# Kernel optimization log

Measured on AMD Instinct MI355X. Metric: run time of the kernel, lower is better.

The kernel has to match this reference:

```python
import jax, jax.numpy as jnp
import numpy as np
from functools import partial

TAU = 2.0
V_TH = 1.0
T_STEPS = 10
SG_ALPHA = 4.0  # spikingjelly surrogate.Sigmoid default

@jax.custom_vjp
def spike(x):
    # Heaviside: 1 where x >= 0 (spikingjelly heaviside semantics)
    return (x >= 0).astype(x.dtype)

def _spike_fwd(x):
    return spike(x), x

def _spike_bwd(x, g):
    s = jax.nn.sigmoid(SG_ALPHA * x)
    return (g * SG_ALPHA * s * (1.0 - s),)

spike.defvjp(_spike_fwd, _spike_bwd)

def setup_inputs() -> dict:
    key = jax.random.key(0)
    ks = jax.random.split(key, 7)
    B, D_IN, H, A = 4096, 2048, 2048, 5
    def lin(k, fan_in, shape):
        bound = 1.0 / np.sqrt(fan_in)
        return jax.random.uniform(k, shape, jnp.float32, -bound, bound)
    return {
        "x": jax.random.normal(ks[0], (B, D_IN), jnp.float32),
        "W_in": lin(ks[1], D_IN, (D_IN, H)),
        "b_in": lin(ks[2], D_IN, (H,)),
        "W_snn": lin(ks[3], H, (H, H)),
        "b_snn": lin(ks[4], H, (H,)),
        "W_out": lin(ks[5], H, (H, A)),
        "b_out": lin(ks[6], H, (A,)),
    }

def lif_step(v, cur):
    # decay_input=True, v_reset=0: v <- v + (I - v)/tau; hard reset with detached spike
    v = v + (cur - v) / TAU
    s = spike(v - V_TH)
    v = (1.0 - jax.lax.stop_gradient(s)) * v
    return v, s

def reference(x, W_in, b_in, W_snn, b_snn, W_out, b_out):
    # input projection [B, H]
    h = x @ W_in + b_in
    # RSNNBlock: fc(h) is the same every timestep; LIF state carries across T steps
    cur = h @ W_snn + b_snn
    v0 = jnp.zeros_like(cur)
    _, spikes = jax.lax.scan(lambda v, _: lif_step(v, cur), v0, None, length=T_STEPS)
    rate = spikes.mean(axis=0)  # [B, H], mean firing rate
    # output head + single-step output LIF (fresh state v=0)
    pre = rate @ W_out + b_out  # [B, A]
    v_out, s_out = lif_step(jnp.zeros_like(pre), pre)
    return s_out
```

## Files before the change

### kernel.cpp

```cpp
#include <hip/hip_runtime.h>
#include <hip/hip_bf16.h>

static constexpr int BATCH = 4096;
static constexpr int DIN   = 2048;
static constexpr int HDIM  = 2048;
static constexpr int ADIM  = 5;

typedef __attribute__((ext_vector_type(8))) short short8;
typedef __attribute__((ext_vector_type(4))) float floatx4;

__device__ __forceinline__ unsigned short f2bf(float f) {
  unsigned int u = __float_as_uint(f);
  unsigned int r = (u + 0x7fffu + ((u >> 16) & 1u)) >> 16;
  return (unsigned short)r;
}
__device__ __forceinline__ float bf2f(unsigned short u) {
  return __uint_as_float(((unsigned int)u) << 16);
}

__global__ __launch_bounds__(256) void k_prep(const float* __restrict__ x,
                                              const float* __restrict__ W_in,
                                              const float* __restrict__ W_snn,
                                              unsigned short* __restrict__ xb,
                                              unsigned short* __restrict__ WinT,
                                              unsigned short* __restrict__ WsnT) {
  __shared__ float tl[32][33];
  const int b = blockIdx.x;
  if (b < 8192) {
    const int i = b * 256 + threadIdx.x;
    float4 v = ((const float4*)x)[i];
    ushort4 o;
    o.x = f2bf(v.x); o.y = f2bf(v.y); o.z = f2bf(v.z); o.w = f2bf(v.w);
    ((ushort4*)xb)[i] = o;
  } else {
    int bi = b - 8192;
    const float* src;
    unsigned short* dst;
    if (bi < 4096) { src = W_in; dst = WinT; }
    else           { src = W_snn; dst = WsnT; bi -= 4096; }
    const int bx = bi & 63, by = bi >> 6;
    const int c0 = bx * 32, r0 = by * 32;
    const int tx = threadIdx.x & 31, ty = threadIdx.x >> 5;
    #pragma unroll
    for (int s = 0; s < 32; s += 8)
      tl[ty + s][tx] = src[(size_t)(r0 + ty + s) * 2048 + (c0 + tx)];
    __syncthreads();
    #pragma unroll
    for (int s = 0; s < 32; s += 8)
      dst[(size_t)(c0 + ty + s) * 2048 + (r0 + tx)] = f2bf(tl[tx][ty + s]);
  }
}

template <int MODE>
__global__ __launch_bounds__(256, 2) void k_gemm(const unsigned short* __restrict__ Ag,
                                                 const unsigned short* __restrict__ BTg,
                                                 const float* __restrict__ bias,
                                                 unsigned short* __restrict__ outb,
                                                 int M, int N, int K) {
  constexpr int BK = 64;
  __shared__ unsigned short smem[2][16384];

  const int nbn = N / 128;
  const int nwg = gridDim.x;
  const int wg  = blockIdx.x;
  const int cpx = nwg >> 3;
  const int swz = (wg & 7) * cpx + (wg >> 3);
  const int bm = swz / nbn, bn = swz % nbn;
  const int m0 = bm * 128, n0 = bn * 128;

  const int t = threadIdx.x;
  const int l = t & 63;
  const int w = t >> 6;
  const int wc  = w & 1;
  const int kkh = w >> 1;

  const int srow = t >> 3;
  const int sg = (((t & 7) ^ (srow & 7)) << 3);
  const unsigned short* gA = Ag + (size_t)(m0 + srow) * K + sg;
  const unsigned short* gB = BTg + (size_t)(n0 + srow) * K + sg;

  const int NT = K / BK;

  auto stage = [&](int tt) {
    const int kt = tt * BK;
    char* base = (char*)&smem[tt & 1][0];
    #pragma unroll
    for (int j = 0; j < 4; ++j)
      __builtin_amdgcn_global_load_lds(
          (const __attribute__((address_space(1))) void*)(gA + (size_t)j * 32 * K + kt),
          (__attribute__((address_space(3))) void*)(base + t * 16 + j * 4096), 16, 0, 0);
    #pragma unroll
    for (int j = 0; j < 4; ++j)
      __builtin_amdgcn_global_load_lds(
          (const __attribute__((address_space(1))) void*)(gB + (size_t)j * 32 * K + kt),
          (__attribute__((address_space(3))) void*)(base + 16384 + t * 16 + j * 4096), 16, 0, 0);
  };

  const int soff = (((kkh << 2) | (l >> 4)) ^ (l & 7)) << 4;
  const int rA0 = (l & 15) * 128;
  const int rB0 = (wc * 64 + (l & 15)) * 128;

  floatx4 acc[8][4] = {};

  stage(0);
  __syncthreads();

  for (int tt = 0; tt < NT; ++tt) {
    if (tt + 1 < NT) stage(tt + 1);
    const char* Ab = (const char*)&smem[tt & 1][0];
    const char* Bb = Ab + 32768;
    short8 bf[4];
    #pragma unroll
    for (int j = 0; j < 4; ++j)
      bf[j] = *(const short8*)(Bb + rB0 + j * 2048 + soff);
    {
      short8 af[4];
      #pragma unroll
      for (int i = 0; i < 4; ++i)
        af[i] = *(const short8*)(Ab + rA0 + i * 2048 + soff);
      #pragma unroll
      for (int i = 0; i < 4; ++i)
        #pragma unroll
        for (int j = 0; j < 4; ++j)
          acc[i][j] = __builtin_amdgcn_mfma_f32_16x16x32_bf16(af[i], bf[j],
                                                              acc[i][j], 0, 0, 0);
    }
    {
      short8 af[4];
      #pragma unroll
      for (int i = 0; i < 4; ++i)
        af[i] = *(const short8*)(Ab + rA0 + (i + 4) * 2048 + soff);
      #pragma unroll
      for (int i = 0; i < 4; ++i)
        #pragma unroll
        for (int j = 0; j < 4; ++j)
          acc[i + 4][j] = __builtin_amdgcn_mfma_f32_16x16x32_bf16(af[i], bf[j],
                                                                  acc[i + 4][j], 0, 0, 0);
    }
    __syncthreads();
  }

  floatx4* xch = (floatx4*)&smem[0][0];
  if (kkh == 1) {
    #pragma unroll
    for (int i = 0; i < 8; ++i)
      #pragma unroll
      for (int j = 0; j < 4; ++j)
        xch[wc * 2048 + (i * 4 + j) * 64 + l] = acc[i][j];
  }
  __syncthreads();
  if (kkh == 0) {
    const int crow = m0 + ((l >> 4) << 2);
    const int ccol = n0 + wc * 64 + (l & 15);
    #pragma unroll
    for (int j = 0; j < 4; ++j) {
      const int col = ccol + j * 16;
      const float bv = bias[col];
      #pragma unroll
      for (int i = 0; i < 8; ++i) {
        floatx4 a = acc[i][j];
        floatx4 o = xch[wc * 2048 + (i * 4 + j) * 64 + l];
        const int row = crow + i * 16;
        #pragma unroll
        for (int r = 0; r < 4; ++r) {
          float v = a[r] + o[r] + bv;
          if (MODE == 1) {
            v = (v >= 2.0f)                ? 10.f
              : (v >= 1.3333333333333333f) ? 5.f
              : (v >= 1.1428571428571428f) ? 3.f
              : (v >= 1.0322580645161290f) ? 2.f
              : (v >= 1.0009775171065494f) ? 1.f : 0.f;
          }
          outb[(size_t)(row + r) * N + col] = f2bf(v);
        }
      }
    }
  }
}

__global__ __launch_bounds__(256) void k_head(const unsigned short* __restrict__ cntb,
                                              const float* __restrict__ Wout,
                                              const float* __restrict__ bout,
                                              float* __restrict__ out) {
  __shared__ float Wl[HDIM * ADIM];
  const int t = threadIdx.x;
  for (int i = t; i < HDIM * ADIM; i += 256) Wl[i] = Wout[i];
  __syncthreads();
  const int w = t >> 6, l = t & 63;
  const int row = blockIdx.x * 4 + w;
  const unsigned short* rp = cntb + (size_t)row * HDIM;
  float acc[ADIM] = {};
  #pragma unroll
  for (int it = 0; it < 4; ++it) {
    const int k0 = it * 512 + l * 8;
    short8 v = *(const short8*)(rp + k0);
    #pragma unroll
    for (int jj = 0; jj < 8; ++jj) {
      const float c = bf2f((unsigned short)v[jj]);
      const int k = k0 + jj;
      #pragma unroll
      for (int a = 0; a < ADIM; ++a) acc[a] += c * Wl[k * ADIM + a];
    }
  }
  #pragma unroll
  for (int a = 0; a < ADIM; ++a)
    #pragma unroll
    for (int off = 32; off >= 1; off >>= 1)
      acc[a] += __shfl_down(acc[a], off, 64);
  if (l == 0) {
    #pragma unroll
    for (int a = 0; a < ADIM; ++a) {
      const float pre = acc[a] * 0.1f + bout[a];
      const float vout = pre * 0.5f;
      out[(size_t)row * ADIM + a] = (vout - 1.0f >= 0.0f) ? 1.0f : 0.0f;
    }
  }
}

extern "C" void kernel_launch(void* const* d_in, const int* in_sizes, int n_in,
                              void* d_out, int out_size, void* d_ws, size_t ws_size,
                              hipStream_t stream) {
  const float* x     = (const float*)d_in[0];
  const float* W_in  = (const float*)d_in[1];
  const float* b_in  = (const float*)d_in[2];
  const float* W_snn = (const float*)d_in[3];
  const float* b_snn = (const float*)d_in[4];
  const float* W_out = (const float*)d_in[5];
  const float* b_out = (const float*)d_in[6];
  float* out = (float*)d_out;

  char* ws = (char*)d_ws;
  unsigned short* xb   = (unsigned short*)(ws);
  unsigned short* WinT = (unsigned short*)(ws + (size_t)16 * 1024 * 1024);
  unsigned short* WsnT = (unsigned short*)(ws + (size_t)24 * 1024 * 1024);
  unsigned short* hb   = (unsigned short*)(ws + (size_t)32 * 1024 * 1024);
  unsigned short* cntb = xb;

  k_prep<<<16384, 256, 0, stream>>>(x, W_in, W_snn, xb, WinT, WsnT);

  const int gblk = (BATCH / 128) * (HDIM / 128);
  k_gemm<0><<<gblk, 256, 0, stream>>>(xb, WinT, b_in, hb, BATCH, HDIM, DIN);

  k_gemm<1><<<gblk, 256, 0, stream>>>(hb, WsnT, b_snn, cntb, BATCH, HDIM, HDIM);

  k_head<<<BATCH / 4, 256, 0, stream>>>(cntb, W_out, b_out, out);
}
```

Baseline: 199.3 us.

## Enlarge GEMM tiles to 256x128 with triple-buffered LDS pipeline, bigger transpose tiles

The GEMM now uses 512-thread blocks covering 256x128 output tiles and keeps three LDS buffers, so loads run two stages ahead and each step waits only through partial vmcnt waits and raw barriers. The weight transpose-and-convert kernel moves to 64x64 tiles, and the head kernel handles four rows per wave to cut the number of blocks and repeated W_out LDS fills. The aim is better operand reuse, fewer exposed load waits, and less launch and staging overhead. In exchange it uses 144KB of LDS per block, which may limit occupancy to a single block per CU despite the launch bound of 2.

Result: slower. 208.4 us (+4.6%).

```diff
diff --git a/kernel.cpp b/kernel.cpp
--- a/kernel.cpp
+++ b/kernel.cpp
@@ -24,7 +24,7 @@
                                               unsigned short* __restrict__ xb,
                                               unsigned short* __restrict__ WinT,
                                               unsigned short* __restrict__ WsnT) {
-  __shared__ float tl[32][33];
+  __shared__ float tl[64][65];
   const int b = blockIdx.x;
   if (b < 8192) {
     const int i = b * 256 + threadIdx.x;
@@ -36,29 +36,29 @@
     int bi = b - 8192;
     const float* src;
     unsigned short* dst;
-    if (bi < 4096) { src = W_in; dst = WinT; }
-    else           { src = W_snn; dst = WsnT; bi -= 4096; }
-    const int bx = bi & 63, by = bi >> 6;
-    const int c0 = bx * 32, r0 = by * 32;
-    const int tx = threadIdx.x & 31, ty = threadIdx.x >> 5;
-    #pragma unroll
-    for (int s = 0; s < 32; s += 8)
+    if (bi < 1024) { src = W_in; dst = WinT; }
+    else           { src = W_snn; dst = WsnT; bi -= 1024; }
+    const int bx = bi & 31, by = bi >> 5;
+    const int c0 = bx * 64, r0 = by * 64;
+    const int tx = threadIdx.x & 63, ty = threadIdx.x >> 6;
+    #pragma unroll
+    for (int s = 0; s < 64; s += 4)
       tl[ty + s][tx] = src[(size_t)(r0 + ty + s) * 2048 + (c0 + tx)];
     __syncthreads();
     #pragma unroll
-    for (int s = 0; s < 32; s += 8)
+    for (int s = 0; s < 64; s += 4)
       dst[(size_t)(c0 + ty + s) * 2048 + (r0 + tx)] = f2bf(tl[tx][ty + s]);
   }
 }
 
 template <int MODE>
-__global__ __launch_bounds__(256, 2) void k_gemm(const unsigned short* __restrict__ Ag,
+__global__ __launch_bounds__(512, 2) void k_gemm(const unsigned short* __restrict__ Ag,
                                                  const unsigned short* __restrict__ BTg,
                                                  const float* __restrict__ bias,
                                                  unsigned short* __restrict__ outb,
                                                  int M, int N, int K) {
   constexpr int BK = 64;
-  __shared__ unsigned short smem[2][16384];
+  __shared__ unsigned short smem[3][24576];
 
   const int nbn = N / 128;
   const int nwg = gridDim.x;
@@ -66,13 +66,14 @@
   const int cpx = nwg >> 3;
   const int swz = (wg & 7) * cpx + (wg >> 3);
   const int bm = swz / nbn, bn = swz % nbn;
-  const int m0 = bm * 128, n0 = bn * 128;
+  const int m0 = bm * 256, n0 = bn * 128;
 
   const int t = threadIdx.x;
   const int l = t & 63;
   const int w = t >> 6;
-  const int wc  = w & 1;
-  const int kkh = w >> 1;
+  const int wc   = w & 1;
+  const int wrow = (w >> 1) & 1;
+  const int kkh  = w >> 2;
 
   const int srow = t >> 3;
   const int sg = (((t & 7) ^ (srow & 7)) << 3);
@@ -81,43 +82,48 @@
 
   const int NT = K / BK;
 
-  auto stage = [&](int tt) {
+  auto stage = [&](int tt, int buf) {
     const int kt = tt * BK;
-    char* base = (char*)&smem[tt & 1][0];
+    char* base = (char*)&smem[buf][0];
     #pragma unroll
     for (int j = 0; j < 4; ++j)
       __builtin_amdgcn_global_load_lds(
-          (const __attribute__((address_space(1))) void*)(gA + (size_t)j * 32 * K + kt),
-          (__attribute__((address_space(3))) void*)(base + t * 16 + j * 4096), 16, 0, 0);
+          (const __attribute__((address_space(1))) void*)(gA + (size_t)j * 64 * K + kt),
+          (__attribute__((address_space(3))) void*)(base + t * 16 + j * 8192), 16, 0, 0);
+    #pragma unroll
+    for (int j = 0; j < 2; ++j)
+      __builtin_amdgcn_global_load_lds(
+          (const __attribute__((address_space(1))) void*)(gB + (size_t)j * 64 * K + kt),
+          (__attribute__((address_space(3))) void*)(base + 32768 + t * 16 + j * 8192), 16, 0, 0);
+  };
+
+  const int soff = (((kkh << 2) | (l >> 4)) ^ (l & 7)) << 4;
+  const int rA0 = (wrow * 128 + (l & 15)) * 128 + soff;
+  const int rB0 = 32768 + (wc * 64 + (l & 15)) * 128 + soff;
+
+  floatx4 acc[8][4] = {};
+
+  stage(0, 0);
+  stage(1, 1);
+  asm volatile("s_waitcnt vmcnt(6)" ::: "memory");
+  __builtin_amdgcn_s_barrier();
+
+  int cur = 0;
+  for (int tt = 0; tt < NT; ++tt) {
+    const char* Ab = (const char*)&smem[cur][0];
+    short8 bf[4];
     #pragma unroll
     for (int j = 0; j < 4; ++j)
-      __builtin_amdgcn_global_load_lds(
-          (const __attribute__((address_space(1))) void*)(gB + (size_t)j * 32 * K + kt),
-          (__attribute__((address_space(3))) void*)(base + 16384 + t * 16 + j * 4096), 16, 0, 0);
-  };
-
-  const int soff = (((kkh << 2) | (l >> 4)) ^ (l & 7)) << 4;
-  const int rA0 = (l & 15) * 128;
-  const int rB0 = (wc * 64 + (l & 15)) * 128;
-
-  floatx4 acc[8][4] = {};
-
-  stage(0);
-  __syncthreads();
-
-  for (int tt = 0; tt < NT; ++tt) {
-    if (tt + 1 < NT) stage(tt + 1);
-    const char* Ab = (const char*)&smem[tt & 1][0];
-    const char* Bb = Ab + 32768;
-    short8 bf[4];
-    #pragma unroll
-    for (int j = 0; j < 4; ++j)
-      bf[j] = *(const short8*)(Bb + rB0 + j * 2048 + soff);
+      bf[j] = *(const short8*)(Ab + rB0 + j * 2048);
+    if (tt + 2 < NT) {
+      int b2 = cur + 2; if (b2 >= 3) b2 -= 3;
+      stage(tt + 2, b2);
+    }
     {
       short8 af[4];
       #pragma unroll
       for (int i = 0; i < 4; ++i)
-        af[i] = *(const short8*)(Ab + rA0 + i * 2048 + soff);
+        af[i] = *(const short8*)(Ab + rA0 + i * 2048);
       #pragma unroll
       for (int i = 0; i < 4; ++i)
         #pragma unroll
@@ -129,7 +135,7 @@
       short8 af[4];
       #pragma unroll
       for (int i = 0; i < 4; ++i)
-        af[i] = *(const short8*)(Ab + rA0 + (i + 4) * 2048 + soff);
+        af[i] = *(const short8*)(Ab + rA0 + (i + 4) * 2048);
       #pragma unroll
       for (int i = 0; i < 4; ++i)
         #pragma unroll
@@ -137,20 +143,26 @@
           acc[i + 4][j] = __builtin_amdgcn_mfma_f32_16x16x32_bf16(af[i], bf[j],
                                                                   acc[i + 4][j], 0, 0, 0);
     }
-    __syncthreads();
-  }
-
+    if (tt + 1 < NT) {
+      if (tt + 2 < NT) asm volatile("s_waitcnt vmcnt(6)" ::: "memory");
+      else             asm volatile("s_waitcnt vmcnt(0)" ::: "memory");
+      __builtin_amdgcn_s_barrier();
+    }
+    cur = (cur == 2) ? 0 : cur + 1;
+  }
+
+  __syncthreads();
   floatx4* xch = (floatx4*)&smem[0][0];
   if (kkh == 1) {
     #pragma unroll
     for (int i = 0; i < 8; ++i)
       #pragma unroll
       for (int j = 0; j < 4; ++j)
-        xch[wc * 2048 + (i * 4 + j) * 64 + l] = acc[i][j];
+        xch[(w & 3) * 2048 + (i * 4 + j) * 64 + l] = acc[i][j];
   }
   __syncthreads();
   if (kkh == 0) {
-    const int crow = m0 + ((l >> 4) << 2);
+    const int crow = m0 + wrow * 128 + ((l >> 4) << 2);
     const int ccol = n0 + wc * 64 + (l & 15);
     #pragma unroll
     for (int j = 0; j < 4; ++j) {
@@ -159,7 +171,7 @@
       #pragma unroll
       for (int i = 0; i < 8; ++i) {
         floatx4 a = acc[i][j];
-        floatx4 o = xch[wc * 2048 + (i * 4 + j) * 64 + l];
+        floatx4 o = xch[w * 2048 + (i * 4 + j) * 64 + l];
         const int row = crow + i * 16;
         #pragma unroll
         for (int r = 0; r < 4; ++r) {
@@ -187,32 +199,35 @@
   for (int i = t; i < HDIM * ADIM; i += 256) Wl[i] = Wout[i];
   __syncthreads();
   const int w = t >> 6, l = t & 63;
-  const int row = blockIdx.x * 4 + w;
-  const unsigned short* rp = cntb + (size_t)row * HDIM;
-  float acc[ADIM] = {};
   #pragma unroll
-  for (int it = 0; it < 4; ++it) {
-    const int k0 = it * 512 + l * 8;
-    short8 v = *(const short8*)(rp + k0);
-    #pragma unroll
-    for (int jj = 0; jj < 8; ++jj) {
-      const float c = bf2f((unsigned short)v[jj]);
-      const int k = k0 + jj;
-      #pragma unroll
-      for (int a = 0; a < ADIM; ++a) acc[a] += c * Wl[k * ADIM + a];
-    }
-  }
-  #pragma unroll
-  for (int a = 0; a < ADIM; ++a)
-    #pragma unroll
-    for (int off = 32; off >= 1; off >>= 1)
-      acc[a] += __shfl_down(acc[a], off, 64);
-  if (l == 0) {
-    #pragma unroll
-    for (int a = 0; a < ADIM; ++a) {
-      const float pre = acc[a] * 0.1f + bout[a];
-      const float vout = pre * 0.5f;
-      out[(size_t)row * ADIM + a] = (vout - 1.0f >= 0.0f) ? 1.0f : 0.0f;
+  for (int rr = 0; rr < 4; ++rr) {
+    const int row = blockIdx.x * 16 + w * 4 + rr;
+    const unsigned short* rp = cntb + (size_t)row * HDIM;
+    float acc[ADIM] = {};
+    #pragma unroll
+    for (int it = 0; it < 4; ++it) {
+      const int k0 = it * 512 + l * 8;
+      short8 v = *(const short8*)(rp + k0);
+      #pragma unroll
+      for (int jj = 0; jj < 8; ++jj) {
+        const float c = bf2f((unsigned short)v[jj]);
+        const int k = k0 + jj;
+        #pragma unroll
+        for (int a = 0; a < ADIM; ++a) acc[a] += c * Wl[k * ADIM + a];
+      }
+    }
+    #pragma unroll
+    for (int a = 0; a < ADIM; ++a)
+      #pragma unroll
+      for (int off = 32; off >= 1; off >>= 1)
+        acc[a] += __shfl_down(acc[a], off, 64);
+    if (l == 0) {
+      #pragma unroll
+      for (int a = 0; a < ADIM; ++a) {
+        const float pre = acc[a] * 0.1f + bout[a];
+        const float vout = pre * 0.5f;
+        out[(size_t)row * ADIM + a] = (vout - 1.0f >= 0.0f) ? 1.0f : 0.0f;
+      }
     }
   }
 }
@@ -236,12 +251,12 @@
   unsigned short* hb   = (unsigned short*)(ws + (size_t)32 * 1024 * 1024);
   unsigned short* cntb = xb;
 
-  k_prep<<<16384, 256, 0, stream>>>(x, W_in, W_snn, xb, WinT, WsnT);
-
-  const int gblk = (BATCH / 128) * (HDIM / 128);
-  k_gemm<0><<<gblk, 256, 0, stream>>>(xb, WinT, b_in, hb, BATCH, HDIM, DIN);
-
-  k_gemm<1><<<gblk, 256, 0, stream>>>(hb, WsnT, b_snn, cntb, BATCH, HDIM, HDIM);
-
-  k_head<<<BATCH / 4, 256, 0, stream>>>(cntb, W_out, b_out, out);
-}
+  k_prep<<<10240, 256, 0, stream>>>(x, W_in, W_snn, xb, WinT, WsnT);
+
+  const int gblk = (BATCH / 256) * (HDIM / 128);
+  k_gemm<0><<<gblk, 512, 0, stream>>>(xb, WinT, b_in, hb, BATCH, HDIM, DIN);
+
+  k_gemm<1><<<gblk, 512, 0, stream>>>(hb, WsnT, b_snn, cntb, BATCH, HDIM, HDIM);
+
+  k_head<<<BATCH / 16, 256, 0, stream>>>(cntb, W_out, b_out, out);
+}
```
